# Optimization experiments

Measured on AMD Instinct MI355X. Metric: run time of the kernel, lower is better.

## Reference

```python
import jax, jax.numpy as jnp
import numpy as np

N = 4096
INPUT_SIZE = 768
DICT_SIZE = 16384
TOP_K = 64


def setup_inputs() -> dict:
    key = jax.random.key(0)
    k1, k2, k3 = jax.random.split(key, 3)
    x = jax.random.normal(k1, (N, INPUT_SIZE), dtype=jnp.float32)
    W_enc = jax.random.normal(k2, (INPUT_SIZE, DICT_SIZE), dtype=jnp.float32) * (1.0 / np.sqrt(INPUT_SIZE))
    b_enc = jax.random.normal(k3, (DICT_SIZE,), dtype=jnp.float32) * 0.01
    return {"x": x, "W_enc": W_enc, "b_enc": b_enc, "top_k": TOP_K}


def reference(x, W_enc, b_enc, top_k):
    # pre_acts = relu(x @ W + b): [N, dict_size]
    pre_acts = jax.nn.relu(jnp.matmul(x, W_enc) + b_enc)
    flat = pre_acts.reshape(-1)  # [N * dict_size]
    k = top_k * x.shape[0]       # global batch-wise budget
    vals, idx = jax.lax.top_k(flat, k)
    out = jnp.zeros_like(flat).at[idx].set(vals)
    return out.reshape(pre_acts.shape)
```

## Files before the change

kernel.cpp:

```cpp
#include <hip/hip_runtime.h>

#define N_ROWS 4096
#define K_DIM  768
#define M_DIM  16384
#define TOTAL  (N_ROWS * M_DIM)
#define K_SEL  262144u
#define NB     8192
#define CAP    8192
#define LOWBITS 0x3F800000u

#define BM 256
#define BN 128
#define BK 32
#define APAD 4

__global__ __launch_bounds__(256) void gemm_relu(const float* __restrict__ A,
                                                 const float* __restrict__ B,
                                                 const float* __restrict__ bias,
                                                 float* __restrict__ C) {
    __shared__ float As[BK][BM + APAD];
    __shared__ float Bs[BK][BN];

    const int tid = threadIdx.x;
    const int wid = tid >> 6;
    const int lane = tid & 63;
    const int tx = tid & 15;
    const int ty = tid >> 4;
    const int row0 = blockIdx.y * BM;
    const int col0 = blockIdx.x * BN;

    float acc[16][8];
#pragma unroll
    for (int i = 0; i < 16; ++i)
#pragma unroll
        for (int j = 0; j < 8; ++j) acc[i][j] = 0.f;

    float4 areg[8];
#pragma unroll
    for (int L = 0; L < 8; ++L) {
        int f = tid + L * 256;
        int r = f >> 3, c4 = (f & 7) << 2;
        areg[L] = *(const float4*)&A[(long long)(row0 + r) * K_DIM + c4];
    }

    for (int k0 = 0; k0 < K_DIM; k0 += BK) {
#pragma unroll
        for (int q = 0; q < 4; ++q) {
            int r = wid * 8 + q * 2 + (lane >> 5);
            const float* src = &B[(long long)(k0 + r) * M_DIM + col0 + ((lane & 31) << 2)];
            __builtin_amdgcn_global_load_lds(
                (const __attribute__((address_space(1))) void*)src,
                (__attribute__((address_space(3))) void*)&Bs[wid * 8 + q * 2][0],
                16, 0, 0);
        }
#pragma unroll
        for (int L = 0; L < 8; ++L) {
            int f = tid + L * 256;
            int r = f >> 3, c4 = (f & 7) << 2;
            As[c4 + 0][r] = areg[L].x; As[c4 + 1][r] = areg[L].y;
            As[c4 + 2][r] = areg[L].z; As[c4 + 3][r] = areg[L].w;
        }
        __syncthreads();

        if (k0 + BK < K_DIM) {
#pragma unroll
            for (int L = 0; L < 8; ++L) {
                int f = tid + L * 256;
                int r = f >> 3, c4 = (f & 7) << 2;
                areg[L] = *(const float4*)&A[(long long)(row0 + r) * K_DIM + (k0 + BK) + c4];
            }
        }

#pragma unroll 4
        for (int kk = 0; kk < BK; ++kk) {
            float4 a0 = *(const float4*)&As[kk][(ty << 4) + 0];
            float4 a1 = *(const float4*)&As[kk][(ty << 4) + 4];
            float4 a2 = *(const float4*)&As[kk][(ty << 4) + 8];
            float4 a3 = *(const float4*)&As[kk][(ty << 4) + 12];
            float4 b0 = *(const float4*)&Bs[kk][tx << 2];
            float4 b1 = *(const float4*)&Bs[kk][64 + (tx << 2)];
            float av[16] = {a0.x, a0.y, a0.z, a0.w, a1.x, a1.y, a1.z, a1.w,
                            a2.x, a2.y, a2.z, a2.w, a3.x, a3.y, a3.z, a3.w};
            float bv[8]  = {b0.x, b0.y, b0.z, b0.w, b1.x, b1.y, b1.z, b1.w};
#pragma unroll
            for (int i = 0; i < 16; ++i)
#pragma unroll
                for (int j = 0; j < 8; ++j) acc[i][j] = fmaf(av[i], bv[j], acc[i][j]);
        }
        __syncthreads();
    }

    float bv[8];
#pragma unroll
    for (int j = 0; j < 4; ++j) {
        bv[j]     = bias[col0 + (tx << 2) + j];
        bv[4 + j] = bias[col0 + 64 + (tx << 2) + j];
    }
#pragma unroll
    for (int i = 0; i < 16; ++i) {
        long long row = row0 + (ty << 4) + i;
        float4 o0, o1;
        o0.x = fmaxf(acc[i][0] + bv[0], 0.f); o0.y = fmaxf(acc[i][1] + bv[1], 0.f);
        o0.z = fmaxf(acc[i][2] + bv[2], 0.f); o0.w = fmaxf(acc[i][3] + bv[3], 0.f);
        o1.x = fmaxf(acc[i][4] + bv[4], 0.f); o1.y = fmaxf(acc[i][5] + bv[5], 0.f);
        o1.z = fmaxf(acc[i][6] + bv[6], 0.f); o1.w = fmaxf(acc[i][7] + bv[7], 0.f);
        *(float4*)&C[row * M_DIM + col0 + (tx << 2)] = o0;
        *(float4*)&C[row * M_DIM + col0 + 64 + (tx << 2)] = o1;
    }
}


__global__ __launch_bounds__(256) void hist1_kernel(const float4* __restrict__ out4,
                                                    unsigned* __restrict__ hist) {
    __shared__ unsigned h[NB];
    for (int i = threadIdx.x; i < NB; i += 256) h[i] = 0u;
    __syncthreads();
    const int stride = gridDim.x * 256;
    for (int i = blockIdx.x * 256 + threadIdx.x; i < TOTAL / 4; i += stride) {
        float4 v = out4[i];
        unsigned b;
        b = __float_as_uint(v.x); if (b >= LOWBITS) atomicAdd(&h[b >> 18], 1u);
        b = __float_as_uint(v.y); if (b >= LOWBITS) atomicAdd(&h[b >> 18], 1u);
        b = __float_as_uint(v.z); if (b >= LOWBITS) atomicAdd(&h[b >> 18], 1u);
        b = __float_as_uint(v.w); if (b >= LOWBITS) atomicAdd(&h[b >> 18], 1u);
    }
    __syncthreads();
    for (int i = threadIdx.x; i < NB; i += 256)
        if (h[i]) atomicAdd(&hist[i], h[i]);
}

__global__ __launch_bounds__(1024) void select_kernel(const unsigned* __restrict__ hist,
                                                      unsigned* __restrict__ meta, int mode) {
    __shared__ unsigned ssum[1024];
    const int t = threadIdx.x;
    const unsigned target = (mode == 0) ? K_SEL : meta[1];
    unsigned loc[8];
    unsigned s = 0;
    const int base = t * 8;
#pragma unroll
    for (int j = 0; j < 8; ++j) { loc[j] = hist[base + j]; s += loc[j]; }
    ssum[t] = s;
    __syncthreads();
    for (int off = 1; off < 1024; off <<= 1) {
        unsigned v = ssum[t];
        unsigned a = (t + off < 1024) ? ssum[t + off] : 0u;
        __syncthreads();
        ssum[t] = v + a;
        __syncthreads();
    }
    const unsigned suffix_excl = ssum[t] - s;
    unsigned cum = suffix_excl;
    for (int j = 7; j >= 0; --j) {
        unsigned Sb1 = cum;
        cum += loc[j];
        if (cum >= target && Sb1 < target) {
            if (mode == 0) { meta[0] = (unsigned)(base + j); meta[1] = target - Sb1; }
            else           { meta[2] = (unsigned)(base + j); meta[3] = target - Sb1; }
        }
    }
}

__global__ __launch_bounds__(256) void hist2_kernel(const float4* __restrict__ out4,
                                                    const unsigned* __restrict__ meta,
                                                    unsigned* __restrict__ hist) {
    __shared__ unsigned h[NB];
    for (int i = threadIdx.x; i < NB; i += 256) h[i] = 0u;
    __syncthreads();
    const unsigned B0 = meta[0];
    const int stride = gridDim.x * 256;
    for (int i = blockIdx.x * 256 + threadIdx.x; i < TOTAL / 4; i += stride) {
        float4 v = out4[i];
        unsigned b;
        b = __float_as_uint(v.x); if ((b >> 18) == B0) atomicAdd(&h[(b >> 5) & 8191u], 1u);
        b = __float_as_uint(v.y); if ((b >> 18) == B0) atomicAdd(&h[(b >> 5) & 8191u], 1u);
        b = __float_as_uint(v.z); if ((b >> 18) == B0) atomicAdd(&h[(b >> 5) & 8191u], 1u);
        b = __float_as_uint(v.w); if ((b >> 18) == B0) atomicAdd(&h[(b >> 5) & 8191u], 1u);
    }
    __syncthreads();
    for (int i = threadIdx.x; i < NB; i += 256)
        if (h[i]) atomicAdd(&hist[i], h[i]);
}

__global__ __launch_bounds__(256) void collect_kernel(const float4* __restrict__ out4,
                                                      unsigned* __restrict__ meta,
                                                      float* __restrict__ cvals,
                                                      unsigned* __restrict__ cidx) {
    const unsigned B0 = meta[0];
    const unsigned B1 = meta[2];
    const int stride = gridDim.x * 256;
    for (int i = blockIdx.x * 256 + threadIdx.x; i < TOTAL / 4; i += stride) {
        float4 v = out4[i];
        const float* vp = &v.x;
#pragma unroll
        for (int j = 0; j < 4; ++j) {
            unsigned b = __float_as_uint(vp[j]);
            if ((b >> 18) == B0 && ((b >> 5) & 8191u) == B1) {
                unsigned p = atomicAdd(&meta[6], 1u);
                if (p < CAP) { cvals[p] = vp[j]; cidx[p] = (unsigned)(i * 4 + j); }
            }
        }
    }
}

__global__ __launch_bounds__(256) void finalize_kernel(const float* __restrict__ cvals,
                                                       const unsigned* __restrict__ cidx,
                                                       unsigned* __restrict__ meta) {
    __shared__ unsigned cnt[32];
    __shared__ unsigned sh_cnt, sh_l, sh_t, sh_prefix;
    __shared__ int sh_lo, sh_hi;
    const int t = threadIdx.x;
    unsigned m = meta[6]; if (m > CAP) m = CAP;
    const unsigned rem2 = meta[3];
    if (t < 32) cnt[t] = 0u;
    __syncthreads();
    for (unsigned i = t; i < m; i += 256) {
        unsigned b = __float_as_uint(cvals[i]);
        atomicAdd(&cnt[b & 31u], 1u);
        if (i == 0) sh_prefix = b & ~31u;
    }
    __syncthreads();
    if (t == 0) {
        unsigned suf = 0; int l = 31;
        for (; l > 0; --l) { if (suf + cnt[l] >= rem2) break; suf += cnt[l]; }
        sh_l = (unsigned)l;
        sh_t = rem2 - suf;
        meta[4] = sh_prefix | (unsigned)l;
        sh_lo = -1; sh_hi = TOTAL - 1;
    }
    __syncthreads();
    const unsigned l = sh_l, tneed = sh_t;
    for (int it = 0; it < 28; ++it) {
        __syncthreads();
        int lo = sh_lo, hi = sh_hi;
        if (lo + 1 < hi) {
            int mid = lo + ((hi - lo) >> 1);
            if (t == 0) sh_cnt = 0u;
            __syncthreads();
            unsigned c = 0;
            for (unsigned i = t; i < m; i += 256) {
                unsigned b = __float_as_uint(cvals[i]);
                if ((b & 31u) == l && cidx[i] <= (unsigned)mid) ++c;
            }
            if (c) atomicAdd(&sh_cnt, c);
            __syncthreads();
            if (t == 0) { if (sh_cnt >= tneed) sh_hi = mid; else sh_lo = mid; }
        }
    }
    __syncthreads();
    if (t == 0) meta[8] = (unsigned)sh_hi;
}

__global__ __launch_bounds__(256) void apply_kernel(float4* __restrict__ out4,
                                                    const unsigned* __restrict__ meta) {
    const unsigned tau = meta[4];
    const unsigned cut = meta[8];
    const int stride = gridDim.x * 256;
    for (int i = blockIdx.x * 256 + threadIdx.x; i < TOTAL / 4; i += stride) {
        float4 v = out4[i];
        unsigned idx0 = (unsigned)i * 4u;
        unsigned b;
        b = __float_as_uint(v.x); if (!(b > tau || (b == tau && idx0 + 0u <= cut))) v.x = 0.f;
        b = __float_as_uint(v.y); if (!(b > tau || (b == tau && idx0 + 1u <= cut))) v.y = 0.f;
        b = __float_as_uint(v.z); if (!(b > tau || (b == tau && idx0 + 2u <= cut))) v.z = 0.f;
        b = __float_as_uint(v.w); if (!(b > tau || (b == tau && idx0 + 3u <= cut))) v.w = 0.f;
        out4[i] = v;
    }
}

extern "C" void kernel_launch(void* const* d_in, const int* in_sizes, int n_in,
                              void* d_out, int out_size, void* d_ws, size_t ws_size,
                              hipStream_t stream) {
    const float* x    = (const float*)d_in[0];
    const float* Wenc = (const float*)d_in[1];
    const float* benc = (const float*)d_in[2];
    float* out = (float*)d_out;

    unsigned char* ws = (unsigned char*)d_ws;
    unsigned* hist1 = (unsigned*)ws;
    unsigned* hist2 = (unsigned*)(ws + 32768);
    unsigned* meta  = (unsigned*)(ws + 65536);
    float*    cvals = (float*)(ws + 65792);
    unsigned* cidx  = (unsigned*)(ws + 65792 + CAP * 4);

    hipMemsetAsync(d_ws, 0, 65792, stream);

    gemm_relu<<<dim3(M_DIM / BN, N_ROWS / BM), 256, 0, stream>>>(x, Wenc, benc, out);

    hist1_kernel<<<2048, 256, 0, stream>>>((const float4*)out, hist1);
    select_kernel<<<1, 1024, 0, stream>>>(hist1, meta, 0);
    hist2_kernel<<<2048, 256, 0, stream>>>((const float4*)out, meta, hist2);
    select_kernel<<<1, 1024, 0, stream>>>(hist2, meta, 1);
    collect_kernel<<<2048, 256, 0, stream>>>((const float4*)out, meta, cvals, cidx);
    finalize_kernel<<<1, 256, 0, stream>>>(cvals, cidx, meta);
    apply_kernel<<<2048, 256, 0, stream>>>((float4*)out, meta);
}
```

Before: 1.640 ms.

## Fuse first-pass histogram into GEMM epilogue and swizzle A tile in LDS

The first radix-select histogram is now built inside the GEMM epilogue. Each block accumulates a 256-bin LDS histogram, offset from the exponent of 1.0 with the top bin clamped, and merges it into global memory with atomics. This removes the separate pass that re-read the whole output and shrinks the first select to 256 bins. The A tile's LDS padding is replaced by an XOR swizzle to avoid bank conflicts without the extra space. In exchange, the epilogue gains per-element LDS atomics, and the clamped top bin assumes the threshold never falls in the highest range.

```diff
diff --git a/kernel.cpp b/kernel.cpp
--- a/kernel.cpp
+++ b/kernel.cpp
@@ -6,19 +6,21 @@
 #define TOTAL  (N_ROWS * M_DIM)
 #define K_SEL  262144u
 #define NB     8192
+#define NB1    256
+#define HBASE  4064u
 #define CAP    8192
 #define LOWBITS 0x3F800000u
 
 #define BM 256
 #define BN 128
 #define BK 32
-#define APAD 4
 
 __global__ __launch_bounds__(256) void gemm_relu(const float* __restrict__ A,
                                                  const float* __restrict__ B,
                                                  const float* __restrict__ bias,
-                                                 float* __restrict__ C) {
-    __shared__ float As[BK][BM + APAD];
+                                                 float* __restrict__ C,
+                                                 unsigned* __restrict__ ghist) {
+    __shared__ float As[BK][BM];
     __shared__ float Bs[BK][BN];
 
     const int tid = threadIdx.x;
@@ -57,8 +59,10 @@
         for (int L = 0; L < 8; ++L) {
             int f = tid + L * 256;
             int r = f >> 3, c4 = (f & 7) << 2;
-            As[c4 + 0][r] = areg[L].x; As[c4 + 1][r] = areg[L].y;
-            As[c4 + 2][r] = areg[L].z; As[c4 + 3][r] = areg[L].w;
+            As[c4 + 0][r ^ ((((c4 + 0) >> 1) & 7) << 2)] = areg[L].x;
+            As[c4 + 1][r ^ ((((c4 + 1) >> 1) & 7) << 2)] = areg[L].y;
+            As[c4 + 2][r ^ ((((c4 + 2) >> 1) & 7) << 2)] = areg[L].z;
+            As[c4 + 3][r ^ ((((c4 + 3) >> 1) & 7) << 2)] = areg[L].w;
         }
         __syncthreads();
 
@@ -73,10 +77,11 @@
 
 #pragma unroll 4
         for (int kk = 0; kk < BK; ++kk) {
-            float4 a0 = *(const float4*)&As[kk][(ty << 4) + 0];
-            float4 a1 = *(const float4*)&As[kk][(ty << 4) + 4];
-            float4 a2 = *(const float4*)&As[kk][(ty << 4) + 8];
-            float4 a3 = *(const float4*)&As[kk][(ty << 4) + 12];
+            const int sk = ((kk >> 1) & 7) << 2;
+            float4 a0 = *(const float4*)&As[kk][((ty << 4) + 0) ^ sk];
+            float4 a1 = *(const float4*)&As[kk][((ty << 4) + 4) ^ sk];
+            float4 a2 = *(const float4*)&As[kk][((ty << 4) + 8) ^ sk];
+            float4 a3 = *(const float4*)&As[kk][((ty << 4) + 12) ^ sk];
             float4 b0 = *(const float4*)&Bs[kk][tx << 2];
             float4 b1 = *(const float4*)&Bs[kk][64 + (tx << 2)];
             float av[16] = {a0.x, a0.y, a0.z, a0.w, a1.x, a1.y, a1.z, a1.w,
@@ -90,6 +95,10 @@
         __syncthreads();
     }
 
+    unsigned* lh = (unsigned*)&As[0][0];
+    lh[tid] = 0u;
+    __syncthreads();
+
     float bv[8];
 #pragma unroll
     for (int j = 0; j < 4; ++j) {
@@ -99,41 +108,53 @@
 #pragma unroll
     for (int i = 0; i < 16; ++i) {
         long long row = row0 + (ty << 4) + i;
-        float4 o0, o1;
-        o0.x = fmaxf(acc[i][0] + bv[0], 0.f); o0.y = fmaxf(acc[i][1] + bv[1], 0.f);
-        o0.z = fmaxf(acc[i][2] + bv[2], 0.f); o0.w = fmaxf(acc[i][3] + bv[3], 0.f);
-        o1.x = fmaxf(acc[i][4] + bv[4], 0.f); o1.y = fmaxf(acc[i][5] + bv[5], 0.f);
-        o1.z = fmaxf(acc[i][6] + bv[6], 0.f); o1.w = fmaxf(acc[i][7] + bv[7], 0.f);
-        *(float4*)&C[row * M_DIM + col0 + (tx << 2)] = o0;
-        *(float4*)&C[row * M_DIM + col0 + 64 + (tx << 2)] = o1;
-    }
-}
-
-
-__global__ __launch_bounds__(256) void hist1_kernel(const float4* __restrict__ out4,
-                                                    unsigned* __restrict__ hist) {
-    __shared__ unsigned h[NB];
-    for (int i = threadIdx.x; i < NB; i += 256) h[i] = 0u;
-    __syncthreads();
-    const int stride = gridDim.x * 256;
-    for (int i = blockIdx.x * 256 + threadIdx.x; i < TOTAL / 4; i += stride) {
-        float4 v = out4[i];
-        unsigned b;
-        b = __float_as_uint(v.x); if (b >= LOWBITS) atomicAdd(&h[b >> 18], 1u);
-        b = __float_as_uint(v.y); if (b >= LOWBITS) atomicAdd(&h[b >> 18], 1u);
-        b = __float_as_uint(v.z); if (b >= LOWBITS) atomicAdd(&h[b >> 18], 1u);
-        b = __float_as_uint(v.w); if (b >= LOWBITS) atomicAdd(&h[b >> 18], 1u);
-    }
-    __syncthreads();
-    for (int i = threadIdx.x; i < NB; i += 256)
-        if (h[i]) atomicAdd(&hist[i], h[i]);
+        float o[8];
+#pragma unroll
+        for (int j = 0; j < 8; ++j) {
+            o[j] = fmaxf(acc[i][j] + bv[j], 0.f);
+            unsigned b = __float_as_uint(o[j]);
+            if (b >= LOWBITS) {
+                unsigned bin = (b >> 18) - HBASE;
+                if (bin > 255u) bin = 255u;
+                atomicAdd(&lh[bin], 1u);
+            }
+        }
+        *(float4*)&C[row * M_DIM + col0 + (tx << 2)]      = make_float4(o[0], o[1], o[2], o[3]);
+        *(float4*)&C[row * M_DIM + col0 + 64 + (tx << 2)] = make_float4(o[4], o[5], o[6], o[7]);
+    }
+    __syncthreads();
+    if (lh[tid]) atomicAdd(&ghist[tid], lh[tid]);
+}
+
+
+
+__global__ __launch_bounds__(NB1) void select0_kernel(const unsigned* __restrict__ hist,
+                                                      unsigned* __restrict__ meta) {
+    __shared__ unsigned ssum[NB1];
+    const int t = threadIdx.x;
+    const unsigned c = hist[t];
+    ssum[t] = c;
+    __syncthreads();
+    for (int off = 1; off < NB1; off <<= 1) {
+        unsigned v = ssum[t];
+        unsigned a = (t + off < NB1) ? ssum[t + off] : 0u;
+        __syncthreads();
+        ssum[t] = v + a;
+        __syncthreads();
+    }
+    const unsigned Sb  = ssum[t];
+    const unsigned Sb1 = Sb - c;
+    if (Sb >= K_SEL && Sb1 < K_SEL) {
+        meta[0] = HBASE + (unsigned)t;
+        meta[1] = K_SEL - Sb1;
+    }
 }
 
 __global__ __launch_bounds__(1024) void select_kernel(const unsigned* __restrict__ hist,
-                                                      unsigned* __restrict__ meta, int mode) {
+                                                      unsigned* __restrict__ meta) {
     __shared__ unsigned ssum[1024];
     const int t = threadIdx.x;
-    const unsigned target = (mode == 0) ? K_SEL : meta[1];
+    const unsigned target = meta[1];
     unsigned loc[8];
     unsigned s = 0;
     const int base = t * 8;
@@ -154,8 +175,8 @@
         unsigned Sb1 = cum;
         cum += loc[j];
         if (cum >= target && Sb1 < target) {
-            if (mode == 0) { meta[0] = (unsigned)(base + j); meta[1] = target - Sb1; }
-            else           { meta[2] = (unsigned)(base + j); meta[3] = target - Sb1; }
+            meta[2] = (unsigned)(base + j);
+            meta[3] = target - Sb1;
         }
     }
 }
@@ -277,19 +298,18 @@
 
     unsigned char* ws = (unsigned char*)d_ws;
     unsigned* hist1 = (unsigned*)ws;
-    unsigned* hist2 = (unsigned*)(ws + 32768);
-    unsigned* meta  = (unsigned*)(ws + 65536);
-    float*    cvals = (float*)(ws + 65792);
-    unsigned* cidx  = (unsigned*)(ws + 65792 + CAP * 4);
-
-    hipMemsetAsync(d_ws, 0, 65792, stream);
-
-    gemm_relu<<<dim3(M_DIM / BN, N_ROWS / BM), 256, 0, stream>>>(x, Wenc, benc, out);
-
-    hist1_kernel<<<2048, 256, 0, stream>>>((const float4*)out, hist1);
-    select_kernel<<<1, 1024, 0, stream>>>(hist1, meta, 0);
+    unsigned* hist2 = (unsigned*)(ws + 1024);
+    unsigned* meta  = (unsigned*)(ws + 1024 + 32768);
+    float*    cvals = (float*)(ws + 34048);
+    unsigned* cidx  = (unsigned*)(ws + 34048 + CAP * 4);
+
+    hipMemsetAsync(d_ws, 0, 34048, stream);
+
+    gemm_relu<<<dim3(M_DIM / BN, N_ROWS / BM), 256, 0, stream>>>(x, Wenc, benc, out, hist1);
+
+    select0_kernel<<<1, NB1, 0, stream>>>(hist1, meta);
     hist2_kernel<<<2048, 256, 0, stream>>>((const float4*)out, meta, hist2);
-    select_kernel<<<1, 1024, 0, stream>>>(hist2, meta, 1);
+    select_kernel<<<1, 1024, 0, stream>>>(hist2, meta);
     collect_kernel<<<2048, 256, 0, stream>>>((const float4*)out, meta, cvals, cidx);
     finalize_kernel<<<1, 256, 0, stream>>>(cvals, cidx, meta);
     apply_kernel<<<2048, 256, 0, stream>>>((float4*)out, meta);
```

Result: slower. 1.797 ms (+9.6%).
